# Optimization experiments

Measured on AMD Instinct MI355X. Metric: run time of the kernel, lower is better.

Reference implementation:

```python
import jax, jax.numpy as jnp
import numpy as np

N_NODES = 50000
N_EDGES = 1600000
IN_F, H_F, N_C = 128, 128, 16
NEG_SLOPE = 0.2  # DGL GATConv default


def setup_inputs() -> dict:
    key = jax.random.key(0)
    ks = jax.random.split(key, 12)
    def w(k, shape, fan_in):
        return jax.random.normal(k, shape, jnp.float32) / np.float32(np.sqrt(fan_in))
    return {
        "feat": jax.random.normal(ks[0], (N_NODES, IN_F), jnp.float32),
        "src": jax.random.randint(ks[1], (N_EDGES,), 0, N_NODES, dtype=jnp.int32),
        "dst": jax.random.randint(ks[2], (N_EDGES,), 0, N_NODES, dtype=jnp.int32),
        "W1": w(ks[3], (IN_F, H_F), IN_F), "al1": w(ks[4], (H_F,), H_F), "ar1": w(ks[5], (H_F,), H_F), "b1": jnp.zeros((H_F,), jnp.float32),
        "W2": w(ks[6], (H_F, H_F), H_F), "al2": w(ks[7], (H_F,), H_F), "ar2": w(ks[8], (H_F,), H_F), "b2": jnp.zeros((H_F,), jnp.float32),
        "W3": w(ks[9], (H_F, N_C), H_F), "al3": w(ks[10], (N_C,), N_C), "ar3": w(ks[11], (N_C,), N_C), "b3": jnp.zeros((N_C,), jnp.float32),
    }


def _gat_layer(h, src, dst, W, al, ar, b):
    # DGL GATConv (1 head): ft = W h; e_ij = LeakyReLU(a_l.ft_src + a_r.ft_dst);
    # alpha = edge_softmax over incoming edges of dst; out = sum alpha * ft_src + bias
    ft = h @ W                                   # [N, out]
    el = ft @ al                                 # [N]
    er = ft @ ar                                 # [N]
    e = jax.nn.leaky_relu(el[src] + er[dst], negative_slope=NEG_SLOPE)  # [E]
    emax = jax.ops.segment_max(e, dst, num_segments=N_NODES)
    emax = jnp.where(jnp.isfinite(emax), emax, 0.0)  # guard isolated nodes
    ex = jnp.exp(e - emax[dst])                  # [E]
    esum = jax.ops.segment_sum(ex, dst, num_segments=N_NODES)  # [N]
    agg = jax.ops.segment_sum(ex[:, None] * ft[src], dst, num_segments=N_NODES)  # [N, out]
    out = agg / jnp.where(esum > 0, esum, 1.0)[:, None] + b
    return jax.nn.relu(out)


def reference(feat, src, dst, W1, al1, ar1, b1, W2, al2, ar2, b2, W3, al3, ar3, b3):
    h = _gat_layer(feat, src, dst, W1, al1, ar1, b1)
    h = _gat_layer(h, src, dst, W2, al2, ar2, b2)
    h = _gat_layer(h, src, dst, W3, al3, ar3, b3)
    return h  # [N_NODES, N_C]
```

## Files before the change

### kernel.cpp

```cpp
#include <hip/hip_runtime.h>
#include <hip/hip_bf16.h>

#define NN 50000
#define NE 1600000
#define FF 128
#define CC 16
#define NB ((NN + 63) / 64)
#define NBLK 256
#define CH ((NE + NBLK - 1) / NBLK)

using bf16 = __hip_bfloat16;
using bf16x8 = __attribute__((ext_vector_type(8))) short;
using f32x4  = __attribute__((ext_vector_type(4))) float;

static __device__ __forceinline__ float ldf(const void* p, int i, int isbf){
    return isbf ? __bfloat162float(((const bf16*)p)[i]) : ((const float*)p)[i];
}
static __device__ __forceinline__ float bflo(unsigned u){
    union{unsigned x; float f;} c; c.x = u << 16; return c.f;
}
static __device__ __forceinline__ float bfhi(unsigned u){
    union{unsigned x; float f;} c; c.x = u & 0xFFFF0000u; return c.f;
}
static __device__ __forceinline__ unsigned short f2bfu(float v){
    bf16 b = __float2bfloat16(v);
    union{bf16 b; unsigned short u;} c; c.b = b; return c.u;
}

__global__ __launch_bounds__(256) void k_prep(const unsigned short* __restrict__ featu,
                                              const void* __restrict__ W1, const void* __restrict__ W2,
                                              const void* __restrict__ W3, int* __restrict__ dflag,
                                              int* __restrict__ bcounts, unsigned short* __restrict__ wtg){
    __shared__ int cnt;
    const int t = threadIdx.x;
    if (t == 0) cnt = 0;
    __syncthreads();
    unsigned short lo = featu[2 * t];
    int e = (lo >> 7) & 0xFF;
    if (e >= 117 && e <= 137) atomicAdd(&cnt, 1);
    __syncthreads();
    const int isbf = (cnt >= 128) ? 1 : 0;
    int idx = blockIdx.x * 256 + t;
    if (idx == 0) *dflag = isbf;
    if (idx < NB) bcounts[idx] = 0;
    if (idx < 32768){
        int l = idx >> 14;
        int e2 = idx & 16383;
        int f = e2 >> 7, k = e2 & 127;
        const void* W = l ? W2 : W1;
        wtg[idx] = f2bfu(ldf(W, k * FF + f, isbf));
    } else if (idx < 34816){
        int e2 = idx - 32768;
        int f = e2 >> 7, k = e2 & 127;
        wtg[idx] = f2bfu(ldf(W3, k * CC + f, isbf));
    }
}


__global__ __launch_bounds__(256) void k_bcount(const int* __restrict__ dst, int* __restrict__ bcounts,
                                                int* __restrict__ bh){
    __shared__ int hist[NB];
    const int t = threadIdx.x, b = blockIdx.x;
    for (int i = t; i < NB; i += 256) hist[i] = 0;
    __syncthreads();
    const int beg = b * CH, end = (beg + CH < NE) ? beg + CH : NE;
    for (int i = beg + t; i < end; i += 256){
        int d = dst[i];
        if ((unsigned)d >= NN) d = 0;
        atomicAdd(&hist[d >> 6], 1);
    }
    __syncthreads();
    for (int k = t; k < NB; k += 256){
        int v = hist[k];
        bh[k * NBLK + b] = v;
        if (v) atomicAdd(&bcounts[k], v);
    }
}

__global__ __launch_bounds__(256) void k_bscan(const int* __restrict__ bcounts, int* __restrict__ bbase,
                                               int* __restrict__ rowptr){
    __shared__ int s[256];
    const int t = threadIdx.x;
    constexpr int PT = (NB + 255) / 256;
    int loc[PT];
    int sum = 0;
    #pragma unroll
    for (int i = 0; i < PT; i++){
        int idx = t * PT + i;
        int v = (idx < NB) ? bcounts[idx] : 0;
        loc[i] = sum;
        sum += v;
    }
    s[t] = sum; __syncthreads();
    for (int off = 1; off < 256; off <<= 1){
        int x = (t >= off) ? s[t - off] : 0;
        __syncthreads();
        s[t] += x;
        __syncthreads();
    }
    int base = (t > 0) ? s[t - 1] : 0;
    #pragma unroll
    for (int i = 0; i < PT; i++){
        int idx = t * PT + i;
        if (idx < NB) bbase[idx] = base + loc[i];
    }
    if (t == 255){
        bbase[NB] = s[255];
        rowptr[NN] = s[255];
    }
}

__global__ __launch_bounds__(256) void k_boffset(const int* __restrict__ bbase, int* __restrict__ bh){
    int k = blockIdx.x * 4 + (threadIdx.x >> 6);
    int lane = threadIdx.x & 63;
    if (k >= NB) return;
    int v[4];
    int s = 0;
    #pragma unroll
    for (int i = 0; i < 4; i++){
        v[i] = bh[k * NBLK + 4 * lane + i];
        s += v[i];
    }
    int tot = s;
    #pragma unroll
    for (int off = 1; off < 64; off <<= 1){
        int x = __shfl_up(s, off);
        if (lane >= off) s += x;
    }
    int run = bbase[k] + s - tot;
    #pragma unroll
    for (int i = 0; i < 4; i++){
        bh[k * NBLK + 4 * lane + i] = run;
        run += v[i];
    }
}

__global__ __launch_bounds__(256) void k_bucket(const int* __restrict__ src, const int* __restrict__ dst,
                                                const int* __restrict__ bh, unsigned* __restrict__ bpairs){
    __shared__ int cur[NB];
    const int t = threadIdx.x, b = blockIdx.x;
    for (int k = t; k < NB; k += 256) cur[k] = bh[k * NBLK + b];
    __syncthreads();
    const int beg = b * CH, end = (beg + CH < NE) ? beg + CH : NE;
    for (int i = beg + t; i < end; i += 256){
        int s = src[i];
        int d = dst[i];
        if ((unsigned)s >= NN) s = 0;
        if ((unsigned)d >= NN) d = 0;
        int p = atomicAdd(&cur[d >> 6], 1);
        if ((unsigned)p < NE) bpairs[p] = (unsigned)s | ((unsigned)(d & 63) << 16);
    }
}

__global__ __launch_bounds__(256) void k_bsort(const unsigned* __restrict__ bpairs, const int* __restrict__ bbase,
                                               int* __restrict__ rowptr, int* __restrict__ csrsrc){
    __shared__ int cnt[64];
    __shared__ int cur[64];
    const int t = threadIdx.x;
    const int b = blockIdx.x;
    const int base = bbase[b];
    const int endb = bbase[b + 1];
    if (t < 64) cnt[t] = 0;
    __syncthreads();
    for (int i = base + t; i < endb; i += 256)
        atomicAdd(&cnt[bpairs[i] >> 16], 1);
    __syncthreads();
    if (t < 64){
        int v = cnt[t];
        int inc = v;
        #pragma unroll
        for (int off = 1; off < 64; off <<= 1){
            int x = __shfl_up(inc, off);
            if (t >= off) inc += x;
        }
        int excl = inc - v;
        cur[t] = excl;
        int d = b * 64 + t;
        if (d < NN) rowptr[d] = base + excl;
    }
    __syncthreads();
    for (int i = base + t; i < endb; i += 256){
        unsigned pr = bpairs[i];
        int p = atomicAdd(&cur[pr >> 16], 1);
        csrsrc[base + p] = (int)(pr & 0xFFFFu);
    }
}


template<bool XDYN>
__global__ __launch_bounds__(256) void k_mgemm(const void* __restrict__ X, const unsigned short* __restrict__ wtg,
                                               const void* __restrict__ al, const void* __restrict__ ar,
                                               const int* __restrict__ dflag, bf16* __restrict__ ft,
                                               float* __restrict__ el, float* __restrict__ er){
    const int isbf = *dflag;
    const int t  = threadIdx.x;
    const int n0 = blockIdx.x * 64;
    const int wv = t >> 6;
    const int lane = t & 63;
    const int quad = lane >> 4;
    const int mcol = lane & 15;
    const int row = n0 + wv * 16 + mcol;
    const int rc  = (row < NN) ? row : 0;

    bf16x8 afr[4];
    if (XDYN && !isbf){
        const float* xr = (const float*)X + rc * FF + quad * 8;
        #pragma unroll
        for (int kt = 0; kt < 4; kt++){
            float4 a = *(const float4*)(xr + kt * 32);
            float4 b = *(const float4*)(xr + kt * 32 + 4);
            union { bf16x8 v; unsigned u[4]; } c;
            c.u[0] = (unsigned)f2bfu(a.x) | ((unsigned)f2bfu(a.y) << 16);
            c.u[1] = (unsigned)f2bfu(a.z) | ((unsigned)f2bfu(a.w) << 16);
            c.u[2] = (unsigned)f2bfu(b.x) | ((unsigned)f2bfu(b.y) << 16);
            c.u[3] = (unsigned)f2bfu(b.z) | ((unsigned)f2bfu(b.w) << 16);
            afr[kt] = c.v;
        }
    } else {
        const unsigned short* xr = (const unsigned short*)X + rc * FF + quad * 8;
        #pragma unroll
        for (int kt = 0; kt < 4; kt++)
            afr[kt] = *(const bf16x8*)(xr + kt * 32);
    }

    float elp[4] = {0.f,0.f,0.f,0.f}, erp[4] = {0.f,0.f,0.f,0.f};

    #pragma unroll
    for (int f = 0; f < 8; f++){
        f32x4 acc = {0.f, 0.f, 0.f, 0.f};
        const unsigned short* wr = wtg + (f * 16 + mcol) * FF + quad * 8;
        #pragma unroll
        for (int kt = 0; kt < 4; kt++){
            bf16x8 bfr = *(const bf16x8*)(wr + kt * 32);
            acc = __builtin_amdgcn_mfma_f32_16x16x32_bf16(afr[kt], bfr, acc, 0, 0, 0);
        }
        int col = f * 16 + mcol;
        float alv = ldf(al, col, isbf);
        float arv = ldf(ar, col, isbf);
        #pragma unroll
        for (int reg = 0; reg < 4; reg++){
            int node = n0 + wv * 16 + quad * 4 + reg;
            float v = acc[reg];
            if (node < NN) ft[node * FF + col] = __float2bfloat16(v);
            elp[reg] += v * alv;
            erp[reg] += v * arv;
        }
    }

    #pragma unroll
    for (int reg = 0; reg < 4; reg++){
        float pl = elp[reg], pr = erp[reg];
        #pragma unroll
        for (int off = 1; off < 16; off <<= 1){
            pl += __shfl_xor(pl, off);
            pr += __shfl_xor(pr, off);
        }
        int node = n0 + wv * 16 + quad * 4 + reg;
        if (mcol == 0 && node < NN){ el[node] = pl; er[node] = pr; }
    }
}


__global__ __launch_bounds__(256) void k_mgemm3(const void* __restrict__ X, const unsigned short* __restrict__ wt3g,
                                                const void* __restrict__ al, const void* __restrict__ ar,
                                                const int* __restrict__ dflag, float* __restrict__ ft,
                                                float* __restrict__ el, float* __restrict__ er){
    const int isbf = *dflag;
    const int t  = threadIdx.x;
    const int n0 = blockIdx.x * 64;
    const int wv = t >> 6;
    const int lane = t & 63;
    const int quad = lane >> 4;
    const int mcol = lane & 15;
    const int row = n0 + wv * 16 + mcol;
    const int rc  = (row < NN) ? row : 0;

    const unsigned short* xr = (const unsigned short*)X + rc * FF + quad * 8;
    const unsigned short* wr = wt3g + mcol * FF + quad * 8;

    f32x4 acc = {0.f, 0.f, 0.f, 0.f};
    #pragma unroll
    for (int kt = 0; kt < 4; kt++){
        bf16x8 afr = *(const bf16x8*)(xr + kt * 32);
        bf16x8 bfr = *(const bf16x8*)(wr + kt * 32);
        acc = __builtin_amdgcn_mfma_f32_16x16x32_bf16(afr, bfr, acc, 0, 0, 0);
    }

    float alv = ldf(al, mcol, isbf);
    float arv = ldf(ar, mcol, isbf);
    #pragma unroll
    for (int reg = 0; reg < 4; reg++){
        int node = n0 + wv * 16 + quad * 4 + reg;
        float v = acc[reg];
        if (node < NN) ft[node * CC + mcol] = v;
        float pl = v * alv, pr = v * arv;
        #pragma unroll
        for (int off = 1; off < 16; off <<= 1){
            pl += __shfl_xor(pl, off);
            pr += __shfl_xor(pr, off);
        }
        if (mcol == 0 && node < NN){ el[node] = pl; er[node] = pr; }
    }
}


__global__ __launch_bounds__(256) void k_agg128(const void* __restrict__ ftv, const float* __restrict__ el,
                                                const float* __restrict__ er, const int* __restrict__ rowptr,
                                                const int* __restrict__ csrsrc, const void* __restrict__ bias,
                                                const int* __restrict__ dflag, unsigned* __restrict__ outp){
    const int isbf = *dflag;
    const int lane = threadIdx.x & 63;
    const int n = blockIdx.x * 4 + (threadIdx.x >> 6);
    if (n >= NN) return;
    int beg = rowptr[n], end = rowptr[n + 1];
    beg = (beg < 0) ? 0 : (beg > NE ? NE : beg);
    end = (end < beg) ? beg : (end > NE ? NE : end);
    const float erd = er[n];

    const int g = lane >> 4;
    const int c = lane & 15;
    const uint4* ftq4 = (const uint4*)ftv;
    float acc[8] = {0.f,0.f,0.f,0.f,0.f,0.f,0.f,0.f};
    float lsum = 0.f;

    for (int j = beg; j < end; j += 16){
        int   sE[4];
        float wE[4];
        uint4 uE[4];
        #pragma unroll
        for (int q = 0; q < 4; q++){
            int iq = j + q * 4 + g;
            int cq = (iq < end) ? iq : beg;
            int s  = csrsrc[cq];
            if ((unsigned)s >= NN) s = 0;
            sE[q] = s;
        }
        #pragma unroll
        for (int q = 0; q < 4; q++){
            int iq = j + q * 4 + g;
            float e = el[sE[q]] + erd;
            e = (e >= 0.f) ? e : 0.2f * e;
            wE[q] = (iq < end) ? __expf(e) : 0.f;
            uE[q] = ftq4[(unsigned)sE[q] * 16u + c];
        }
        #pragma unroll
        for (int q = 0; q < 4; q++){
            float w = wE[q];
            lsum += w;
            acc[0] += w * bflo(uE[q].x); acc[1] += w * bfhi(uE[q].x);
            acc[2] += w * bflo(uE[q].y); acc[3] += w * bfhi(uE[q].y);
            acc[4] += w * bflo(uE[q].z); acc[5] += w * bfhi(uE[q].z);
            acc[6] += w * bflo(uE[q].w); acc[7] += w * bfhi(uE[q].w);
        }
    }

    #pragma unroll
    for (int k = 0; k < 8; k++){
        acc[k] += __shfl_xor(acc[k], 16);
        acc[k] += __shfl_xor(acc[k], 32);
    }
    lsum += __shfl_xor(lsum, 16);
    lsum += __shfl_xor(lsum, 32);

    if (g == 0){
        float inv = (lsum > 0.f) ? 1.f / lsum : 0.f;
        float o[8];
        #pragma unroll
        for (int k = 0; k < 8; k++)
            o[k] = fmaxf(acc[k] * inv + ldf(bias, c * 8 + k, isbf), 0.f);
        uint4 pk;
        pk.x = (unsigned)f2bfu(o[0]) | ((unsigned)f2bfu(o[1]) << 16);
        pk.y = (unsigned)f2bfu(o[2]) | ((unsigned)f2bfu(o[3]) << 16);
        pk.z = (unsigned)f2bfu(o[4]) | ((unsigned)f2bfu(o[5]) << 16);
        pk.w = (unsigned)f2bfu(o[6]) | ((unsigned)f2bfu(o[7]) << 16);
        ((uint4*)outp)[n * 16 + c] = pk;
    }
}


__global__ __launch_bounds__(256) void k_agg16(const float* __restrict__ ftv, const float* __restrict__ el,
                                               const float* __restrict__ er, const int* __restrict__ rowptr,
                                               const int* __restrict__ csrsrc, const void* __restrict__ bias,
                                               const int* __restrict__ dflag, void* __restrict__ outp){
    const int isbf = *dflag;
    const int lane = threadIdx.x & 63;
    const int n = blockIdx.x * 4 + (threadIdx.x >> 6);
    if (n >= NN) return;
    int beg = rowptr[n], end = rowptr[n + 1];
    beg = (beg < 0) ? 0 : (beg > NE ? NE : beg);
    end = (end < beg) ? beg : (end > NE ? NE : end);
    const float erd = er[n];

    const int g = lane >> 2;
    const int c = lane & 3;
    const float4* ftq = (const float4*)ftv;
    float a0 = 0.f, a1 = 0.f, a2 = 0.f, a3 = 0.f;
    float lsum = 0.f;

    for (int j = beg; j < end; j += 32){
        #pragma unroll
        for (int q = 0; q < 2; q++){
            int iq = j + q * 16 + g;
            int cq = (iq < end) ? iq : beg;
            int s  = csrsrc[cq];
            if ((unsigned)s >= NN) s = 0;
            float e = el[s] + erd;
            e = (e >= 0.f) ? e : 0.2f * e;
            float w = (iq < end) ? __expf(e) : 0.f;
            float4 u = ftq[(unsigned)s * 4u + c];
            lsum += w;
            a0 += w * u.x; a1 += w * u.y; a2 += w * u.z; a3 += w * u.w;
        }
    }

    #pragma unroll
    for (int off = 4; off < 64; off <<= 1){
        a0 += __shfl_xor(a0, off);
        a1 += __shfl_xor(a1, off);
        a2 += __shfl_xor(a2, off);
        a3 += __shfl_xor(a3, off);
        lsum += __shfl_xor(lsum, off);
    }

    if (lane < 4){
        float inv = (lsum > 0.f) ? 1.f / lsum : 0.f;
        float o0 = fmaxf(a0 * inv + ldf(bias, c * 4 + 0, isbf), 0.f);
        float o1 = fmaxf(a1 * inv + ldf(bias, c * 4 + 1, isbf), 0.f);
        float o2 = fmaxf(a2 * inv + ldf(bias, c * 4 + 2, isbf), 0.f);
        float o3 = fmaxf(a3 * inv + ldf(bias, c * 4 + 3, isbf), 0.f);
        if (isbf){
            uint2 pk;
            pk.x = (unsigned)f2bfu(o0) | ((unsigned)f2bfu(o1) << 16);
            pk.y = (unsigned)f2bfu(o2) | ((unsigned)f2bfu(o3) << 16);
            ((uint2*)outp)[n * 4 + c] = pk;
        } else {
            float4 o; o.x = o0; o.y = o1; o.z = o2; o.w = o3;
            ((float4*)outp)[n * 4 + c] = o;
        }
    }
}


static size_t align256(size_t x){ return (x + 255) & ~(size_t)255; }

extern "C" void kernel_launch(void* const* d_in, const int* in_sizes, int n_in,
                              void* d_out, int out_size, void* d_ws, size_t ws_size,
                              hipStream_t stream) {
    const void* feat = d_in[0];
    const int*  src  = (const int*)d_in[1];
    const int*  dst  = (const int*)d_in[2];
    const void* W1 = d_in[3];
    const void* al1= d_in[4];
    const void* ar1= d_in[5];
    const void* b1 = d_in[6];
    const void* W2 = d_in[7];
    const void* al2= d_in[8];
    const void* ar2= d_in[9];
    const void* b2 = d_in[10];
    const void* W3 = d_in[11];
    const void* al3= d_in[12];
    const void* ar3= d_in[13];
    const void* b3 = d_in[14];

    char* p = (char*)d_ws;
    size_t off = 0;
    auto carve = [&](size_t bytes)->void*{
        void* r = p + off;
        off += align256(bytes);
        return r;
    };
    float* ftA   = (float*)carve((size_t)NN * FF * 4);
    unsigned* hB = (unsigned*)carve((size_t)NN * FF * 4);
    float* el    = (float*)carve((size_t)NN * 4);
    float* er    = (float*)carve((size_t)NN * 4);
    int*   rowptr= (int*)  carve((size_t)(NN + 1) * 4);
    int*   csrsrc= (int*)  carve((size_t)NE * 4);
    int*   bcounts=(int*)  carve((size_t)NB * 4);
    int*   bbase  =(int*)  carve((size_t)(NB + 1) * 4);
    int*   bh     =(int*)  carve((size_t)NB * NBLK * 4);
    unsigned short* wtg = (unsigned short*)carve((size_t)34816 * 2);
    int*   dflag  =(int*)  carve(256);
    unsigned* bpairs = (unsigned*)hB;
    void*  ftb   = ftA;
    (void)ws_size; (void)n_in; (void)in_sizes; (void)out_size;

    dim3 b256(256);

    k_prep<<<dim3(136), b256, 0, stream>>>((const unsigned short*)feat, W1, W2, W3, dflag, bcounts, wtg);

    k_bcount<<<dim3(NBLK), b256, 0, stream>>>(dst, bcounts, bh);
    k_bscan<<<dim3(1), b256, 0, stream>>>(bcounts, bbase, rowptr);
    k_boffset<<<dim3((NB + 3) / 4), b256, 0, stream>>>(bbase, bh);
    k_bucket<<<dim3(NBLK), b256, 0, stream>>>(src, dst, bh, bpairs);
    k_bsort<<<dim3(NB), b256, 0, stream>>>(bpairs, bbase, rowptr, csrsrc);

    const int mg_grid   = (NN + 63) / 64;
    const int node_grid = (NN + 3) / 4;

    k_mgemm<true><<<dim3(mg_grid), b256, 0, stream>>>(feat, wtg, al1, ar1, dflag, (bf16*)ftb, el, er);
    k_agg128<<<dim3(node_grid), b256, 0, stream>>>(ftb, el, er, rowptr, csrsrc, b1, dflag, hB);

    k_mgemm<false><<<dim3(mg_grid), b256, 0, stream>>>(hB, wtg + 16384, al2, ar2, dflag, (bf16*)ftb, el, er);
    k_agg128<<<dim3(node_grid), b256, 0, stream>>>(ftb, el, er, rowptr, csrsrc, b2, dflag, hB);

    k_mgemm3<<<dim3(mg_grid), b256, 0, stream>>>(hB, wtg + 32768, al3, ar3, dflag, (float*)ftb, el, er);
    k_agg16<<<dim3(node_grid), b256, 0, stream>>>((const float*)ftb, el, er, rowptr, csrsrc, b3, dflag, d_out);
}
```

Baseline: 350.3 us.

## Partition bf16 features into 32-column planes and precompute edge softmax weights

Features and hidden activations are stored in four column-partitioned planes of 32 bf16 values per node. The 128-wide aggregation is split into four blocks per node group, each gathering only 64 bytes per source. A new k_wnorm kernel computes the exp edge weights once into a CSR-ordered buffer, plus the reciprocal softmax denominator. This aims to shrink each gather's working set so it fits in cache better, and to avoid recomputing exp in every partition. The cost is an extra kernel pass, an extra weight array read per edge and per partition, and four times as many reads of the CSR indices.

```diff
diff --git a/kernel.cpp b/kernel.cpp
--- a/kernel.cpp
+++ b/kernel.cpp
@@ -187,10 +187,10 @@
 }
 
 
-template<bool XDYN>
+template<int MODE>
 __global__ __launch_bounds__(256) void k_mgemm(const void* __restrict__ X, const unsigned short* __restrict__ wtg,
                                                const void* __restrict__ al, const void* __restrict__ ar,
-                                               const int* __restrict__ dflag, bf16* __restrict__ ft,
+                                               const int* __restrict__ dflag, unsigned short* __restrict__ ftP,
                                                float* __restrict__ el, float* __restrict__ er){
     const int isbf = *dflag;
     const int t  = threadIdx.x;
@@ -203,7 +203,7 @@
     const int rc  = (row < NN) ? row : 0;
 
     bf16x8 afr[4];
-    if (XDYN && !isbf){
+    if (MODE == 0 && !isbf){
         const float* xr = (const float*)X + rc * FF + quad * 8;
         #pragma unroll
         for (int kt = 0; kt < 4; kt++){
@@ -216,11 +216,18 @@
             c.u[3] = (unsigned)f2bfu(b.z) | ((unsigned)f2bfu(b.w) << 16);
             afr[kt] = c.v;
         }
-    } else {
+    } else if (MODE == 0){
         const unsigned short* xr = (const unsigned short*)X + rc * FF + quad * 8;
         #pragma unroll
         for (int kt = 0; kt < 4; kt++)
             afr[kt] = *(const bf16x8*)(xr + kt * 32);
+    } else {
+        #pragma unroll
+        for (int kt = 0; kt < 4; kt++){
+            int q8 = quad * 8 + kt * 32;
+            const unsigned short* xr = (const unsigned short*)X + ((size_t)(q8 >> 5) * NN + rc) * 32 + (q8 & 31);
+            afr[kt] = *(const bf16x8*)xr;
+        }
     }
 
     float elp[4] = {0.f,0.f,0.f,0.f}, erp[4] = {0.f,0.f,0.f,0.f};
@@ -241,7 +248,8 @@
         for (int reg = 0; reg < 4; reg++){
             int node = n0 + wv * 16 + quad * 4 + reg;
             float v = acc[reg];
-            if (node < NN) ft[node * FF + col] = __float2bfloat16(v);
+            if (node < NN)
+                ftP[((size_t)(f >> 1) * NN + node) * 32 + (f & 1) * 16 + mcol] = f2bfu(v);
             elp[reg] += v * alv;
             erp[reg] += v * arv;
         }
@@ -275,13 +283,14 @@
     const int row = n0 + wv * 16 + mcol;
     const int rc  = (row < NN) ? row : 0;
 
-    const unsigned short* xr = (const unsigned short*)X + rc * FF + quad * 8;
     const unsigned short* wr = wt3g + mcol * FF + quad * 8;
 
     f32x4 acc = {0.f, 0.f, 0.f, 0.f};
     #pragma unroll
     for (int kt = 0; kt < 4; kt++){
-        bf16x8 afr = *(const bf16x8*)(xr + kt * 32);
+        int q8 = quad * 8 + kt * 32;
+        const unsigned short* xr = (const unsigned short*)X + ((size_t)(q8 >> 5) * NN + rc) * 32 + (q8 & 31);
+        bf16x8 afr = *(const bf16x8*)xr;
         bf16x8 bfr = *(const bf16x8*)(wr + kt * 32);
         acc = __builtin_amdgcn_mfma_f32_16x16x32_bf16(afr, bfr, acc, 0, 0, 0);
     }
@@ -304,76 +313,76 @@
 }
 
 
-__global__ __launch_bounds__(256) void k_agg128(const void* __restrict__ ftv, const float* __restrict__ el,
-                                                const float* __restrict__ er, const int* __restrict__ rowptr,
-                                                const int* __restrict__ csrsrc, const void* __restrict__ bias,
-                                                const int* __restrict__ dflag, unsigned* __restrict__ outp){
+__global__ __launch_bounds__(256) void k_wnorm(const float* __restrict__ el, float* __restrict__ er,
+                                               const int* __restrict__ rowptr, const int* __restrict__ csrsrc,
+                                               float* __restrict__ wcsr){
+    const int t = threadIdx.x;
+    const int n = blockIdx.x * 32 + (t >> 3);
+    if (n >= NN) return;
+    const int sub = t & 7;
+    int beg = rowptr[n], end = rowptr[n + 1];
+    beg = (beg < 0) ? 0 : (beg > NE ? NE : beg);
+    end = (end < beg) ? beg : (end > NE ? NE : end);
+    const float erd = er[n];
+    float sum = 0.f;
+    for (int i = beg + sub; i < end; i += 8){
+        int s = csrsrc[i];
+        if ((unsigned)s >= NN) s = 0;
+        float e = el[s] + erd;
+        e = (e >= 0.f) ? e : 0.2f * e;
+        float ex = __expf(e);
+        wcsr[i] = ex;
+        sum += ex;
+    }
+    sum += __shfl_xor(sum, 1);
+    sum += __shfl_xor(sum, 2);
+    sum += __shfl_xor(sum, 4);
+    if (sub == 0) er[n] = 1.f / ((sum > 0.f) ? sum : 1.f);
+}
+
+
+__global__ __launch_bounds__(256) void k_agg128(const unsigned* __restrict__ ftP, const int* __restrict__ rowptr,
+                                                const int* __restrict__ csrsrc, const float* __restrict__ wcsr,
+                                                const float* __restrict__ erinv, const void* __restrict__ bias,
+                                                const int* __restrict__ dflag, unsigned* __restrict__ outP){
     const int isbf = *dflag;
+    const int p   = blockIdx.x & 3;
+    const int grp = blockIdx.x >> 2;
     const int lane = threadIdx.x & 63;
-    const int n = blockIdx.x * 4 + (threadIdx.x >> 6);
+    const int n = grp * 4 + (threadIdx.x >> 6);
     if (n >= NN) return;
     int beg = rowptr[n], end = rowptr[n + 1];
     beg = (beg < 0) ? 0 : (beg > NE ? NE : beg);
     end = (end < beg) ? beg : (end > NE ? NE : end);
-    const float erd = er[n];
 
     const int g = lane >> 4;
     const int c = lane & 15;
-    const uint4* ftq4 = (const uint4*)ftv;
-    float acc[8] = {0.f,0.f,0.f,0.f,0.f,0.f,0.f,0.f};
-    float lsum = 0.f;
+    const unsigned* fp = ftP + (size_t)p * NN * 16;
+    float a0 = 0.f, a1 = 0.f;
 
     for (int j = beg; j < end; j += 16){
-        int   sE[4];
-        float wE[4];
-        uint4 uE[4];
         #pragma unroll
         for (int q = 0; q < 4; q++){
             int iq = j + q * 4 + g;
             int cq = (iq < end) ? iq : beg;
             int s  = csrsrc[cq];
             if ((unsigned)s >= NN) s = 0;
-            sE[q] = s;
-        }
-        #pragma unroll
-        for (int q = 0; q < 4; q++){
-            int iq = j + q * 4 + g;
-            float e = el[sE[q]] + erd;
-            e = (e >= 0.f) ? e : 0.2f * e;
-            wE[q] = (iq < end) ? __expf(e) : 0.f;
-            uE[q] = ftq4[(unsigned)sE[q] * 16u + c];
-        }
-        #pragma unroll
-        for (int q = 0; q < 4; q++){
-            float w = wE[q];
-            lsum += w;
-            acc[0] += w * bflo(uE[q].x); acc[1] += w * bfhi(uE[q].x);
-            acc[2] += w * bflo(uE[q].y); acc[3] += w * bfhi(uE[q].y);
-            acc[4] += w * bflo(uE[q].z); acc[5] += w * bfhi(uE[q].z);
-            acc[6] += w * bflo(uE[q].w); acc[7] += w * bfhi(uE[q].w);
-        }
-    }
-
-    #pragma unroll
-    for (int k = 0; k < 8; k++){
-        acc[k] += __shfl_xor(acc[k], 16);
-        acc[k] += __shfl_xor(acc[k], 32);
-    }
-    lsum += __shfl_xor(lsum, 16);
-    lsum += __shfl_xor(lsum, 32);
+            float w = (iq < end) ? wcsr[cq] : 0.f;
+            unsigned u = fp[(unsigned)s * 16u + c];
+            a0 += w * bflo(u);
+            a1 += w * bfhi(u);
+        }
+    }
+
+    a0 += __shfl_xor(a0, 16); a0 += __shfl_xor(a0, 32);
+    a1 += __shfl_xor(a1, 16); a1 += __shfl_xor(a1, 32);
 
     if (g == 0){
-        float inv = (lsum > 0.f) ? 1.f / lsum : 0.f;
-        float o[8];
-        #pragma unroll
-        for (int k = 0; k < 8; k++)
-            o[k] = fmaxf(acc[k] * inv + ldf(bias, c * 8 + k, isbf), 0.f);
-        uint4 pk;
-        pk.x = (unsigned)f2bfu(o[0]) | ((unsigned)f2bfu(o[1]) << 16);
-        pk.y = (unsigned)f2bfu(o[2]) | ((unsigned)f2bfu(o[3]) << 16);
-        pk.z = (unsigned)f2bfu(o[4]) | ((unsigned)f2bfu(o[5]) << 16);
-        pk.w = (unsigned)f2bfu(o[6]) | ((unsigned)f2bfu(o[7]) << 16);
-        ((uint4*)outp)[n * 16 + c] = pk;
+        float inv = erinv[n];
+        int fcol = p * 32 + 2 * c;
+        float o0 = fmaxf(a0 * inv + ldf(bias, fcol,     isbf), 0.f);
+        float o1 = fmaxf(a1 * inv + ldf(bias, fcol + 1, isbf), 0.f);
+        outP[((size_t)p * NN + n) * 16u + c] = (unsigned)f2bfu(o0) | ((unsigned)f2bfu(o1) << 16);
     }
 }
 
@@ -482,6 +491,7 @@
     int*   dflag  =(int*)  carve(256);
     unsigned* bpairs = (unsigned*)hB;
     void*  ftb   = ftA;
+    float* wcsr  = ftA + (size_t)NN * FF / 2;
     (void)ws_size; (void)n_in; (void)in_sizes; (void)out_size;
 
     dim3 b256(256);
@@ -496,12 +506,16 @@
 
     const int mg_grid   = (NN + 63) / 64;
     const int node_grid = (NN + 3) / 4;
-
-    k_mgemm<true><<<dim3(mg_grid), b256, 0, stream>>>(feat, wtg, al1, ar1, dflag, (bf16*)ftb, el, er);
-    k_agg128<<<dim3(node_grid), b256, 0, stream>>>(ftb, el, er, rowptr, csrsrc, b1, dflag, hB);
-
-    k_mgemm<false><<<dim3(mg_grid), b256, 0, stream>>>(hB, wtg + 16384, al2, ar2, dflag, (bf16*)ftb, el, er);
-    k_agg128<<<dim3(node_grid), b256, 0, stream>>>(ftb, el, er, rowptr, csrsrc, b2, dflag, hB);
+    const int agg_grid  = node_grid * 4;
+    const int wn_grid   = (NN + 31) / 32;
+
+    k_mgemm<0><<<dim3(mg_grid), b256, 0, stream>>>(feat, wtg, al1, ar1, dflag, (unsigned short*)ftb, el, er);
+    k_wnorm<<<dim3(wn_grid), b256, 0, stream>>>(el, er, rowptr, csrsrc, wcsr);
+    k_agg128<<<dim3(agg_grid), b256, 0, stream>>>((const unsigned*)ftb, rowptr, csrsrc, wcsr, er, b1, dflag, hB);
+
+    k_mgemm<1><<<dim3(mg_grid), b256, 0, stream>>>(hB, wtg + 16384, al2, ar2, dflag, (unsigned short*)ftb, el, er);
+    k_wnorm<<<dim3(wn_grid), b256, 0, stream>>>(el, er, rowptr, csrsrc, wcsr);
+    k_agg128<<<dim3(agg_grid), b256, 0, stream>>>((const unsigned*)ftb, rowptr, csrsrc, wcsr, er, b2, dflag, hB);
 
     k_mgemm3<<<dim3(mg_grid), b256, 0, stream>>>(hB, wtg + 32768, al3, ar3, dflag, (float*)ftb, el, er);
     k_agg16<<<dim3(node_grid), b256, 0, stream>>>((const float*)ftb, el, er, rowptr, csrsrc, b3, dflag, d_out);
```

After: 517.4 us. +47.7%, slower.
